# Optimization experiments

Hardware: AMD Instinct MI355X
Metric: run time of the kernel (lower is better)

Reference implementation:

```python
import jax, jax.numpy as jnp
import numpy as np

N = 100000      # num nodes
E = 1600000     # num edges (avg degree 16)
D_IN = 64
D_OUT = 32
NEG_SLOPE = 0.01  # torch LeakyReLU default


def setup_inputs() -> dict:
    key = jax.random.key(0)
    k1, k2, k3, k4 = jax.random.split(key, 4)
    x = jax.random.normal(k1, (N, D_IN), dtype=jnp.float32)
    edge_index = jax.random.randint(k2, (2, E), 0, N, dtype=jnp.int32)
    # GCNConv linear weights (glorot-ish init) and biases
    W1 = jax.random.normal(k3, (D_IN, D_IN), dtype=jnp.float32) / np.float32(np.sqrt(D_IN))
    b1 = jnp.zeros((D_IN,), dtype=jnp.float32)
    W2 = jax.random.normal(k4, (D_IN, D_OUT), dtype=jnp.float32) / np.float32(np.sqrt(D_IN))
    b2 = jnp.zeros((D_OUT,), dtype=jnp.float32)
    return {"x": x, "edge_index": edge_index, "W1": W1, "b1": b1, "W2": W2, "b2": b2}


def reference(x, edge_index, W1, b1, W2, b2):
    # PyG GCNConv default: add self-loops, symmetric normalization D^-1/2 (A+I) D^-1/2
    loops = jnp.arange(N, dtype=edge_index.dtype)
    src = jnp.concatenate([edge_index[0], loops])  # [E+N]
    dst = jnp.concatenate([edge_index[1], loops])  # [E+N]
    deg = jax.ops.segment_sum(jnp.ones(src.shape[0], jnp.float32), dst, num_segments=N)
    dinv = jax.lax.rsqrt(deg)  # deg >= 1 due to self-loops
    norm = dinv[src] * dinv[dst]  # [E+N]

    def gcn_conv(h, W, b):
        h = h @ W                          # [N, d_out]
        msg = h[src] * norm[:, None]       # gather + normalize  [E+N, d_out]
        return jax.ops.segment_sum(msg, dst, num_segments=N) + b  # scatter-add

    h = gcn_conv(x, W1, b1)
    h = jnp.where(h > 0, h, NEG_SLOPE * h)  # LeakyReLU
    return gcn_conv(h, W2, b2)
```

## Files before the change

### kernel.cpp

```cpp
#include <hip/hip_runtime.h>

#define N_NODES 100000
#define N_EDGES 1600000
#define DIN 64
#define DOUT 32
#define NEG_SLOPE 0.01f
#define NBUCK 196
#define CAP 12288
#define CH 4096
#define NB1 ((N_EDGES + CH - 1) / CH)

__device__ inline unsigned short f2bf(float f) {
    unsigned int u = __float_as_uint(f);
    unsigned int r = (u + 0x7fffu + ((u >> 16) & 1u)) >> 16;
    return (unsigned short)r;
}
__device__ inline float bflo(unsigned int p) { return __uint_as_float(p << 16); }
__device__ inline float bfhi(unsigned int p) { return __uint_as_float(p & 0xffff0000u); }
#define NTL(p) __builtin_nontemporal_load(p)

__device__ inline void addpack4(float* a, uint4 r) {
    a[0] += bflo(r.x); a[1] += bfhi(r.x);
    a[2] += bflo(r.y); a[3] += bfhi(r.y);
    a[4] += bflo(r.z); a[5] += bfhi(r.z);
    a[6] += bflo(r.w); a[7] += bfhi(r.w);
}
__device__ inline void addpack2(float* a, uint2 r) {
    a[0] += bflo(r.x); a[1] += bfhi(r.x);
    a[2] += bflo(r.y); a[3] += bfhi(r.y);
}

__global__ __launch_bounds__(256) void binpass1_kernel(const int* __restrict__ src,
                                                       const int* __restrict__ dst,
                                                       int* __restrict__ bucketfill,
                                                       unsigned int* __restrict__ staging2) {
    __shared__ int histw[4][NBUCK];
    __shared__ int base[NBUCK];
    __shared__ int tot[NBUCK];
    __shared__ int gbase[NBUCK];
    __shared__ int scanbuf[256];
    __shared__ unsigned int sorted[CH];
    int tid = threadIdx.x;
    int w = tid >> 6;
    int b = blockIdx.x;
    for (int t = tid; t < 4 * NBUCK; t += 256) ((int*)histw)[t] = 0;
    __syncthreads();

    int e0 = b * CH + tid;
    int bk[16];
    int rk[16];
    unsigned int pay[16];
#pragma unroll
    for (int i = 0; i < 16; ++i) {
        int e = e0 + i * 256;
        if (e < N_EDGES) {
            int d = NTL(&dst[e]);
            int s = NTL(&src[e]);
            bk[i] = d >> 9;
            pay[i] = (unsigned int)s | ((unsigned int)(d & 511) << 17);
            rk[i] = atomicAdd(&histw[w][bk[i]], 1);
        } else {
            bk[i] = -1;
        }
    }
    __syncthreads();
    int v = 0;
    if (tid < NBUCK) {
        int h0 = histw[0][tid], h1 = histw[1][tid], h2 = histw[2][tid], h3 = histw[3][tid];
        histw[0][tid] = 0;
        histw[1][tid] = h0;
        histw[2][tid] = h0 + h1;
        histw[3][tid] = h0 + h1 + h2;
        v = h0 + h1 + h2 + h3;
        tot[tid] = v;
    }
    scanbuf[tid] = (tid < NBUCK) ? v : 0;
    __syncthreads();
    for (int off = 1; off < 256; off <<= 1) {
        int a = scanbuf[tid];
        int add = (tid >= off) ? scanbuf[tid - off] : 0;
        __syncthreads();
        scanbuf[tid] = a + add;
        __syncthreads();
    }
    if (tid < NBUCK) {
        base[tid] = scanbuf[tid] - v;
        gbase[tid] = v ? atomicAdd(&bucketfill[tid], v) : 0;
    }
    __syncthreads();
#pragma unroll
    for (int i = 0; i < 16; ++i) {
        if (bk[i] >= 0) sorted[base[bk[i]] + histw[w][bk[i]] + rk[i]] = pay[i];
    }
    __syncthreads();
    int wv = tid >> 6, ln = tid & 63;
    for (int k = wv; k < NBUCK; k += 4) {
        int h = tot[k];
        int b0 = base[k];
        int g0 = gbase[k];
        unsigned int* dp = staging2 + (size_t)k * CAP;
        for (int i = ln; i < h; i += 64)
            if (g0 + i < CAP) dp[g0 + i] = sorted[b0 + i];
    }
}

__global__ __launch_bounds__(1024) void binpass2_kernel(const unsigned int* __restrict__ staging2,
                                                        const int* __restrict__ bucketfill,
                                                        int* __restrict__ rowptr,
                                                        float* __restrict__ dinv,
                                                        int* __restrict__ colsrc) {
    __shared__ int hist[512];
    __shared__ int posl[512];
    __shared__ int sh[512];
    __shared__ int red[4];
    int k = blockIdx.x;
    int tid = threadIdx.x;
    int base_node = k << 9;
    int nn = min(512, N_NODES - base_node);
    int len = min(bucketfill[k], CAP);

    if (tid < 256) {
        int v = (tid < k) ? bucketfill[tid] : 0;
#pragma unroll
        for (int off = 32; off; off >>= 1) v += __shfl_down(v, off);
        if ((tid & 63) == 0) red[tid >> 6] = v;
    }
    if (tid < 512) hist[tid] = 0;
    __syncthreads();
    int bbase = red[0] + red[1] + red[2] + red[3];
    const unsigned int* stg = staging2 + (size_t)k * CAP;

    for (int i = tid; i < len; i += 1024) atomicAdd(&hist[stg[i] >> 17], 1);
    __syncthreads();

    int v = 0;
    if (tid < 512) { v = hist[tid]; sh[tid] = v; }
    __syncthreads();
    for (int off = 1; off < 512; off <<= 1) {
        int a = 0, add = 0;
        if (tid < 512) { a = sh[tid]; add = (tid >= off) ? sh[tid - off] : 0; }
        __syncthreads();
        if (tid < 512) sh[tid] = a + add;
        __syncthreads();
    }
    if (tid < 512) {
        int excl = sh[tid] - v;
        posl[tid] = bbase + excl;
        if (tid < nn) {
            rowptr[base_node + tid] = bbase + excl;
            dinv[base_node + tid] = rsqrtf((float)(v + 1));
        }
    }
    if (k == NBUCK - 1 && tid == 0) rowptr[N_NODES] = N_EDGES;
    __syncthreads();
    for (int i = tid; i < len; i += 1024) {
        unsigned int pay = stg[i];
        int idx = atomicAdd(&posl[pay >> 17], 1);
        colsrc[idx] = (int)(pay & 0x1FFFFu);
    }
}

__global__ __launch_bounds__(256) void gemm_k64_n64_kernel(const float* __restrict__ X,
                                                           const float* __restrict__ W,
                                                           const float* __restrict__ dinv,
                                                           unsigned short* __restrict__ Hn) {
    __shared__ float Ws[64 * 64];
    __shared__ float Xs[64][65];
    int tid = threadIdx.x;
    int row0 = blockIdx.x * 64;
    {
        const float4* Wv = (const float4*)W;
        float4* Wsv = (float4*)Ws;
#pragma unroll
        for (int i = 0; i < 4; ++i) Wsv[tid + 256 * i] = Wv[tid + 256 * i];
    }
#pragma unroll
    for (int i = 0; i < 4; ++i) {
        int s = tid + i * 256;
        int r = s >> 4, c = (s & 15) * 4;
        int gr = row0 + r;
        float4 xv = (gr < N_NODES) ? *(const float4*)(X + (size_t)gr * 64 + c)
                                   : make_float4(0.f, 0.f, 0.f, 0.f);
        Xs[r][c] = xv.x; Xs[r][c + 1] = xv.y; Xs[r][c + 2] = xv.z; Xs[r][c + 3] = xv.w;
    }
    __syncthreads();

    int c4 = (tid & 15) * 4;
    int r4 = (tid >> 4) * 4;
    float a0[4] = {}, a1[4] = {}, a2[4] = {}, a3[4] = {};
#pragma unroll 8
    for (int k = 0; k < 64; ++k) {
        float4 w = *(const float4*)&Ws[(k << 6) + c4];
        float x0 = Xs[r4][k], x1 = Xs[r4 + 1][k], x2 = Xs[r4 + 2][k], x3 = Xs[r4 + 3][k];
        a0[0] += x0 * w.x; a0[1] += x0 * w.y; a0[2] += x0 * w.z; a0[3] += x0 * w.w;
        a1[0] += x1 * w.x; a1[1] += x1 * w.y; a1[2] += x1 * w.z; a1[3] += x1 * w.w;
        a2[0] += x2 * w.x; a2[1] += x2 * w.y; a2[2] += x2 * w.z; a2[3] += x2 * w.w;
        a3[0] += x3 * w.x; a3[1] += x3 * w.y; a3[2] += x3 * w.z; a3[3] += x3 * w.w;
    }
    float* accs[4] = {a0, a1, a2, a3};
#pragma unroll
    for (int r = 0; r < 4; ++r) {
        int gr = row0 + r4 + r;
        if (gr < N_NODES) {
            float dv = dinv[gr];
            float* a = accs[r];
            unsigned int lo = (unsigned int)f2bf(a[0] * dv) | ((unsigned int)f2bf(a[1] * dv) << 16);
            unsigned int hi = (unsigned int)f2bf(a[2] * dv) | ((unsigned int)f2bf(a[3] * dv) << 16);
            *(uint2*)(Hn + (size_t)gr * 64 + c4) = make_uint2(lo, hi);
        }
    }
}

__global__ void gemm_k64_n32_bf16_kernel(const unsigned short* __restrict__ Xb,
                                         const float* __restrict__ W,
                                         const float* __restrict__ dinv,
                                         unsigned short* __restrict__ Hn) {
    __shared__ float Ws[64 * 32];
    __shared__ float Xs[8][64];
    int tid = threadIdx.x;
    {
        const float4* Wv = (const float4*)W;
        float4* Wsv = (float4*)Ws;
#pragma unroll
        for (int i = 0; i < 2; ++i) Wsv[tid + 256 * i] = Wv[tid + 256 * i];
    }
    int row0 = blockIdx.x * 8;
    {
        unsigned int w = ((const unsigned int*)(Xb + (size_t)row0 * 64))[tid];
        int r = tid >> 5, p = (tid & 31) << 1;
        Xs[r][p] = bflo(w);
        Xs[r][p + 1] = bfhi(w);
    }
    __syncthreads();

    int r = tid >> 5;
    int col = tid & 31;
    float sum = 0.f;
#pragma unroll
    for (int k = 0; k < 64; ++k) sum += Xs[r][k] * Ws[k * 32 + col];
    Hn[(size_t)(row0 + r) * 32 + col] = f2bf(sum * dinv[row0 + r]);
}

__global__ __launch_bounds__(256) void gather64_kernel(
    const unsigned short* __restrict__ Hn, const int* __restrict__ rowptr,
    const int* __restrict__ colsrc, const float* __restrict__ dinv,
    const float* __restrict__ bias, unsigned short* __restrict__ h1b) {
    int gwid = (blockIdx.x * blockDim.x + threadIdx.x) >> 6;
    int lane = threadIdx.x & 63;
    int g = lane >> 3, sl = lane & 7, gb = g << 3;
    int v = gwid * 8 + g;
    if (v >= N_NODES) return;
    int beg = rowptr[v], end = rowptr[v + 1];

    float acc[8], ac2[8];
#pragma unroll
    for (int i = 0; i < 8; ++i) { acc[i] = 0.f; ac2[i] = 0.f; }
    {
        uint4 rw = ((const uint4*)(Hn + (size_t)v * 64))[sl];
        addpack4(acc, rw);
    }
    int t0 = beg;
    for (; t0 + 8 <= end; t0 += 8) {
        int sv = colsrc[t0 + sl];
        uint4 r[8];
#pragma unroll
        for (int t = 0; t < 8; ++t) {
            int s = __shfl(sv, gb + t);
            r[t] = ((const uint4*)(Hn + (size_t)s * 64))[sl];
        }
#pragma unroll
        for (int t = 0; t < 8; t += 2) {
            addpack4(acc, r[t]);
            addpack4(ac2, r[t + 1]);
        }
    }
    if (t0 < end) {
        int sv = (t0 + sl < end) ? colsrc[t0 + sl] : 0;
        int cnt = end - t0;
        int t = 0;
        for (; t + 2 <= cnt; t += 2) {
            int s0 = __shfl(sv, gb + t);
            int s1 = __shfl(sv, gb + t + 1);
            uint4 r0 = ((const uint4*)(Hn + (size_t)s0 * 64))[sl];
            uint4 r1 = ((const uint4*)(Hn + (size_t)s1 * 64))[sl];
            addpack4(acc, r0);
            addpack4(ac2, r1);
        }
        if (t < cnt) {
            int s0 = __shfl(sv, gb + t);
            uint4 r0 = ((const uint4*)(Hn + (size_t)s0 * 64))[sl];
            addpack4(acc, r0);
        }
    }
    float dv = dinv[v];
    float4 b0 = ((const float4*)(bias + sl * 8))[0];
    float4 b1v = ((const float4*)(bias + sl * 8))[1];
    float o[8];
    o[0] = (acc[0] + ac2[0]) * dv + b0.x;  o[1] = (acc[1] + ac2[1]) * dv + b0.y;
    o[2] = (acc[2] + ac2[2]) * dv + b0.z;  o[3] = (acc[3] + ac2[3]) * dv + b0.w;
    o[4] = (acc[4] + ac2[4]) * dv + b1v.x; o[5] = (acc[5] + ac2[5]) * dv + b1v.y;
    o[6] = (acc[6] + ac2[6]) * dv + b1v.z; o[7] = (acc[7] + ac2[7]) * dv + b1v.w;
#pragma unroll
    for (int i = 0; i < 8; ++i) o[i] = o[i] > 0.f ? o[i] : NEG_SLOPE * o[i];
    uint4 pk;
    pk.x = (unsigned int)f2bf(o[0]) | ((unsigned int)f2bf(o[1]) << 16);
    pk.y = (unsigned int)f2bf(o[2]) | ((unsigned int)f2bf(o[3]) << 16);
    pk.z = (unsigned int)f2bf(o[4]) | ((unsigned int)f2bf(o[5]) << 16);
    pk.w = (unsigned int)f2bf(o[6]) | ((unsigned int)f2bf(o[7]) << 16);
    *(uint4*)(h1b + (size_t)v * 64 + sl * 8) = pk;
}

__global__ __launch_bounds__(256) void gather32_kernel(
    const unsigned short* __restrict__ Hn, const int* __restrict__ rowptr,
    const int* __restrict__ colsrc, const float* __restrict__ dinv,
    const float* __restrict__ bias, float* __restrict__ out) {
    int gwid = (blockIdx.x * blockDim.x + threadIdx.x) >> 6;
    int lane = threadIdx.x & 63;
    int g = lane >> 3, sl = lane & 7, gb = g << 3;
    int v = gwid * 8 + g;
    if (v >= N_NODES) return;
    int beg = rowptr[v], end = rowptr[v + 1];

    float acc[4], ac2[4];
#pragma unroll
    for (int i = 0; i < 4; ++i) { acc[i] = 0.f; ac2[i] = 0.f; }
    {
        uint2 rw = ((const uint2*)(Hn + (size_t)v * 32))[sl];
        addpack2(acc, rw);
    }
    int t0 = beg;
    for (; t0 + 8 <= end; t0 += 8) {
        int sv = colsrc[t0 + sl];
        uint2 r[8];
#pragma unroll
        for (int t = 0; t < 8; ++t) {
            int s = __shfl(sv, gb + t);
            r[t] = ((const uint2*)(Hn + (size_t)s * 32))[sl];
        }
#pragma unroll
        for (int t = 0; t < 8; t += 2) {
            addpack2(acc, r[t]);
            addpack2(ac2, r[t + 1]);
        }
    }
    if (t0 < end) {
        int sv = (t0 + sl < end) ? colsrc[t0 + sl] : 0;
        int cnt = end - t0;
        int t = 0;
        for (; t + 2 <= cnt; t += 2) {
            int s0 = __shfl(sv, gb + t);
            int s1 = __shfl(sv, gb + t + 1);
            uint2 r0 = ((const uint2*)(Hn + (size_t)s0 * 32))[sl];
            uint2 r1 = ((const uint2*)(Hn + (size_t)s1 * 32))[sl];
            addpack2(acc, r0);
            addpack2(ac2, r1);
        }
        if (t < cnt) {
            int s0 = __shfl(sv, gb + t);
            uint2 r0 = ((const uint2*)(Hn + (size_t)s0 * 32))[sl];
            addpack2(acc, r0);
        }
    }
    float dv = dinv[v];
    float4 bb = ((const float4*)bias)[sl];
    float o0 = (acc[0] + ac2[0]) * dv + bb.x;
    float o1 = (acc[1] + ac2[1]) * dv + bb.y;
    float o2 = (acc[2] + ac2[2]) * dv + bb.z;
    float o3 = (acc[3] + ac2[3]) * dv + bb.w;
    *(float4*)(out + (size_t)v * 32 + sl * 4) = make_float4(o0, o1, o2, o3);
}

extern "C" void kernel_launch(void* const* d_in, const int* in_sizes, int n_in,
                              void* d_out, int out_size, void* d_ws, size_t ws_size,
                              hipStream_t stream) {
    const float* x = (const float*)d_in[0];
    const int* ei = (const int*)d_in[1];
    const float* W1 = (const float*)d_in[2];
    const float* b1 = (const float*)d_in[3];
    const float* W2 = (const float*)d_in[4];
    const float* b2 = (const float*)d_in[5];
    float* out = (float*)d_out;

    const int* src = ei;
    const int* dst = ei + N_EDGES;

    char* p = (char*)d_ws;
    auto alloc = [&](size_t bytes) { char* r = p; p += (bytes + 255) & ~(size_t)255; return r; };
    float* dinv = (float*)alloc(N_NODES * 4);
    int* rowptr = (int*)alloc((N_NODES + 1) * 4);
    int* bucketfill = (int*)alloc(NBUCK * 4);
    int* colsrc = (int*)alloc((size_t)N_EDGES * 4);
    unsigned short* h1n = (unsigned short*)alloc((size_t)N_NODES * DIN * 2);
    unsigned short* h1b = (unsigned short*)alloc((size_t)N_NODES * DIN * 2);
    unsigned short* h2n = (unsigned short*)alloc((size_t)N_NODES * DOUT * 2);
    unsigned int* staging2 = (unsigned int*)alloc((size_t)NBUCK * CAP * 4);

    hipMemsetAsync(bucketfill, 0, NBUCK * sizeof(int), stream);
    binpass1_kernel<<<NB1, 256, 0, stream>>>(src, dst, bucketfill, staging2);
    binpass2_kernel<<<NBUCK, 1024, 0, stream>>>(staging2, bucketfill, rowptr, dinv, colsrc);

    gemm_k64_n64_kernel<<<(N_NODES + 63) / 64, 256, 0, stream>>>(x, W1, dinv, h1n);

    gather64_kernel<<<(N_NODES / 8 * 64) / 256, 256, 0, stream>>>(
        h1n, rowptr, colsrc, dinv, b1, h1b);

    gemm_k64_n32_bf16_kernel<<<N_NODES / 8, 256, 0, stream>>>(h1b, W2, dinv, h2n);

    gather32_kernel<<<(N_NODES / 8 * 64) / 256, 256, 0, stream>>>(
        h2n, rowptr, colsrc, dinv, b2, out);
}
```

Baseline: 143.9 us.

## Fuse layer-1 aggregation with layer-2 GEMM and stage bucket data in LDS

The layer-1 gather/LeakyReLU kernel now keeps each block's 32 output rows in shared memory and multiplies them by W2 directly, writing the bf16 normalized layer-2 features. This removes the h1b intermediate write/read and one kernel launch. Separately, binpass2 copies each bucket's staged entries into a 48KB LDS buffer once with nontemporal loads instead of reading global memory twice. The large LDS allocation in binpass2 lowers occupancy, and the fused kernel adds a block barrier plus extra LDS use.

After: 128.5 us (median of 2 runs). 1.12x faster.

```diff
diff --git a/kernel.cpp b/kernel.cpp
--- a/kernel.cpp
+++ b/kernel.cpp
@@ -109,6 +109,7 @@
                                                         int* __restrict__ rowptr,
                                                         float* __restrict__ dinv,
                                                         int* __restrict__ colsrc) {
+    __shared__ unsigned int coll[CAP];
     __shared__ int hist[512];
     __shared__ int posl[512];
     __shared__ int sh[512];
@@ -130,7 +131,9 @@
     int bbase = red[0] + red[1] + red[2] + red[3];
     const unsigned int* stg = staging2 + (size_t)k * CAP;
 
-    for (int i = tid; i < len; i += 1024) atomicAdd(&hist[stg[i] >> 17], 1);
+    for (int i = tid; i < len; i += 1024) coll[i] = NTL(&stg[i]);
+    __syncthreads();
+    for (int i = tid; i < len; i += 1024) atomicAdd(&hist[coll[i] >> 17], 1);
     __syncthreads();
 
     int v = 0;
@@ -154,7 +157,7 @@
     if (k == NBUCK - 1 && tid == 0) rowptr[N_NODES] = N_EDGES;
     __syncthreads();
     for (int i = tid; i < len; i += 1024) {
-        unsigned int pay = stg[i];
+        unsigned int pay = coll[i];
         int idx = atomicAdd(&posl[pay >> 17], 1);
         colsrc[idx] = (int)(pay & 0x1FFFFu);
     }
@@ -211,45 +214,26 @@
     }
 }
 
-__global__ void gemm_k64_n32_bf16_kernel(const unsigned short* __restrict__ Xb,
-                                         const float* __restrict__ W,
-                                         const float* __restrict__ dinv,
-                                         unsigned short* __restrict__ Hn) {
-    __shared__ float Ws[64 * 32];
-    __shared__ float Xs[8][64];
+__global__ __launch_bounds__(256) void gather64_fused_kernel(
+    const unsigned short* __restrict__ Hn, const int* __restrict__ rowptr,
+    const int* __restrict__ colsrc, const float* __restrict__ dinv,
+    const float* __restrict__ bias, const float* __restrict__ W2,
+    unsigned short* __restrict__ h2n) {
+    __shared__ float R[32][65];
+    __shared__ float W2s[64][32];
     int tid = threadIdx.x;
     {
-        const float4* Wv = (const float4*)W;
-        float4* Wsv = (float4*)Ws;
+        const float4* Wv = (const float4*)W2;
+        float4* Wsv = (float4*)W2s;
 #pragma unroll
         for (int i = 0; i < 2; ++i) Wsv[tid + 256 * i] = Wv[tid + 256 * i];
     }
-    int row0 = blockIdx.x * 8;
-    {
-        unsigned int w = ((const unsigned int*)(Xb + (size_t)row0 * 64))[tid];
-        int r = tid >> 5, p = (tid & 31) << 1;
-        Xs[r][p] = bflo(w);
-        Xs[r][p + 1] = bfhi(w);
-    }
-    __syncthreads();
-
-    int r = tid >> 5;
-    int col = tid & 31;
-    float sum = 0.f;
-#pragma unroll
-    for (int k = 0; k < 64; ++k) sum += Xs[r][k] * Ws[k * 32 + col];
-    Hn[(size_t)(row0 + r) * 32 + col] = f2bf(sum * dinv[row0 + r]);
-}
-
-__global__ __launch_bounds__(256) void gather64_kernel(
-    const unsigned short* __restrict__ Hn, const int* __restrict__ rowptr,
-    const int* __restrict__ colsrc, const float* __restrict__ dinv,
-    const float* __restrict__ bias, unsigned short* __restrict__ h1b) {
-    int gwid = (blockIdx.x * blockDim.x + threadIdx.x) >> 6;
-    int lane = threadIdx.x & 63;
+
+    int lane = tid & 63;
+    int w = tid >> 6;
     int g = lane >> 3, sl = lane & 7, gb = g << 3;
-    int v = gwid * 8 + g;
-    if (v >= N_NODES) return;
+    int nodeLocal = w * 8 + g;
+    int v = blockIdx.x * 32 + nodeLocal;
     int beg = rowptr[v], end = rowptr[v + 1];
 
     float acc[8], ac2[8];
@@ -302,12 +286,24 @@
     o[6] = (acc[6] + ac2[6]) * dv + b1v.z; o[7] = (acc[7] + ac2[7]) * dv + b1v.w;
 #pragma unroll
     for (int i = 0; i < 8; ++i) o[i] = o[i] > 0.f ? o[i] : NEG_SLOPE * o[i];
-    uint4 pk;
-    pk.x = (unsigned int)f2bf(o[0]) | ((unsigned int)f2bf(o[1]) << 16);
-    pk.y = (unsigned int)f2bf(o[2]) | ((unsigned int)f2bf(o[3]) << 16);
-    pk.z = (unsigned int)f2bf(o[4]) | ((unsigned int)f2bf(o[5]) << 16);
-    pk.w = (unsigned int)f2bf(o[6]) | ((unsigned int)f2bf(o[7]) << 16);
-    *(uint4*)(h1b + (size_t)v * 64 + sl * 8) = pk;
+    *(float4*)&R[nodeLocal][sl * 8] = make_float4(o[0], o[1], o[2], o[3]);
+    *(float4*)&R[nodeLocal][sl * 8 + 4] = make_float4(o[4], o[5], o[6], o[7]);
+    __syncthreads();
+
+    int row = tid >> 3;
+    int c4 = (tid & 7) * 4;
+    float a[4] = {};
+#pragma unroll 8
+    for (int k = 0; k < 64; ++k) {
+        float x = R[row][k];
+        float4 wv = *(const float4*)&W2s[k][c4];
+        a[0] += x * wv.x; a[1] += x * wv.y; a[2] += x * wv.z; a[3] += x * wv.w;
+    }
+    int gv = blockIdx.x * 32 + row;
+    float dv2 = dinv[gv];
+    unsigned int lo = (unsigned int)f2bf(a[0] * dv2) | ((unsigned int)f2bf(a[1] * dv2) << 16);
+    unsigned int hi = (unsigned int)f2bf(a[2] * dv2) | ((unsigned int)f2bf(a[3] * dv2) << 16);
+    *(uint2*)(h2n + (size_t)gv * 32 + c4) = make_uint2(lo, hi);
 }
 
 __global__ __launch_bounds__(256) void gather32_kernel(
@@ -391,7 +387,6 @@
     int* bucketfill = (int*)alloc(NBUCK * 4);
     int* colsrc = (int*)alloc((size_t)N_EDGES * 4);
     unsigned short* h1n = (unsigned short*)alloc((size_t)N_NODES * DIN * 2);
-    unsigned short* h1b = (unsigned short*)alloc((size_t)N_NODES * DIN * 2);
     unsigned short* h2n = (unsigned short*)alloc((size_t)N_NODES * DOUT * 2);
     unsigned int* staging2 = (unsigned int*)alloc((size_t)NBUCK * CAP * 4);
 
@@ -401,10 +396,8 @@
 
     gemm_k64_n64_kernel<<<(N_NODES + 63) / 64, 256, 0, stream>>>(x, W1, dinv, h1n);
 
-    gather64_kernel<<<(N_NODES / 8 * 64) / 256, 256, 0, stream>>>(
-        h1n, rowptr, colsrc, dinv, b1, h1b);
-
-    gemm_k64_n32_bf16_kernel<<<N_NODES / 8, 256, 0, stream>>>(h1b, W2, dinv, h2n);
+    gather64_fused_kernel<<<N_NODES / 32, 256, 0, stream>>>(
+        h1n, rowptr, colsrc, dinv, b1, W2, h2n);
 
     gather32_kernel<<<(N_NODES / 8 * 64) / 256, 256, 0, stream>>>(
         h2n, rowptr, colsrc, dinv, b2, out);
```
